# Optimization experiments

Measured on AMD Instinct MI355X. Metric: run time of the kernel, lower is better.

Reference implementation:

```python
import jax, jax.numpy as jnp
import numpy as np

EMBED_DIM = 1024
NUM_HEADS = 16
HEAD_DIM = EMBED_DIM // NUM_HEADS


def setup_inputs() -> dict:
    key = jax.random.key(0)
    k_x, k_wqkv, k_bqkv, k_wo, k_bo = jax.random.split(key, 5)
    b, n = 2, 2048
    scale_in = 1.0 / np.sqrt(EMBED_DIM)
    return {
        "x": jax.random.normal(k_x, (b, n, EMBED_DIM), dtype=jnp.float32),
        "W_qkv": jax.random.normal(k_wqkv, (EMBED_DIM, 3 * EMBED_DIM), dtype=jnp.float32) * scale_in,
        "b_qkv": jnp.zeros((3 * EMBED_DIM,), dtype=jnp.float32),
        "W_out": jax.random.normal(k_wo, (EMBED_DIM, EMBED_DIM), dtype=jnp.float32) * scale_in,
        "b_out": jnp.zeros((EMBED_DIM,), dtype=jnp.float32),
    }


def _rope_rotate(t, cos, sin):
    # t: [b, h, n, hd]; cos/sin: [1, 1, n, hd//2]
    t1, t2 = jnp.split(t, 2, axis=-1)
    return jnp.concatenate([cos * t1 - sin * t2, sin * t1 + cos * t2], axis=-1)


def reference(x, W_qkv, b_qkv, W_out, b_out):
    b, n, d = x.shape
    h, hd = NUM_HEADS, HEAD_DIM

    qkv = x @ W_qkv + b_qkv                      # [b, n, 3d]
    q, k, v = jnp.split(qkv, 3, axis=-1)
    q, k, v = [t.reshape(b, n, h, hd).transpose(0, 2, 1, 3) for t in (q, k, v)]

    # RoPE tables
    hd2 = hd // 2
    theta = 10000.0 ** (-2.0 * jnp.arange(hd2, dtype=jnp.float32) / hd)
    freqs = jnp.arange(n, dtype=jnp.float32)[:, None] * theta[None, :]  # [n, hd2]
    cos = jnp.cos(freqs)[None, None]
    sin = jnp.sin(freqs)[None, None]
    q = _rope_rotate(q, cos, sin)
    k = _rope_rotate(k, cos, sin)

    scores = jnp.einsum('bhqd,bhkd->bhqk', q, k) / jnp.sqrt(jnp.float32(hd))
    attn = jax.nn.softmax(scores, axis=-1)       # [b, h, n, n]
    out = jnp.einsum('bhqk,bhkd->bhqd', attn, v)
    out = out.transpose(0, 2, 1, 3).reshape(b, n, d)
    return out @ W_out + b_out
```

## Files before the change

kernel.cpp:

```cpp
#include <hip/hip_runtime.h>
#include <hip/hip_bf16.h>
#include <math.h>

#define EMBED 1024
#define NHEAD 16
#define HD 64
#define BATCH 2
#define SEQ 2048
#define MTOT (BATCH * SEQ)
#define QKVN (3 * EMBED)

typedef __attribute__((ext_vector_type(8))) short short8;
typedef __attribute__((ext_vector_type(4))) float f32x4;

typedef __attribute__((address_space(1))) const unsigned int GUI;
typedef __attribute__((address_space(3))) unsigned int LUI;

__device__ __forceinline__ void gload_lds16(const void* src, void* dst) {
  __builtin_amdgcn_global_load_lds((GUI*)src, (LUI*)dst, 16, 0, 0);
}

__device__ __forceinline__ unsigned short f2bf(float f) {
  unsigned u = __builtin_bit_cast(unsigned, f);
  u += 0x7fffu + ((u >> 16) & 1u);
  return (unsigned short)(u >> 16);
}

__device__ __forceinline__ unsigned cvt_pk_bf16(float lo, float hi) {
  unsigned r;
  asm("v_cvt_pk_bf16_f32 %0, %1, %2" : "=v"(r) : "v"(lo), "v"(hi));
  return r;
}

#if __has_builtin(__builtin_amdgcn_exp2f)
#define EXP2(x) __builtin_amdgcn_exp2f(x)
#else
#define EXP2(x) __builtin_exp2f(x)
#endif

#define QSCALE 0.1803368801111191f


__global__ __launch_bounds__(256) void k_cvt(const float* __restrict__ in,
                                             unsigned short* __restrict__ out, int n4) {
  int i = blockIdx.x * 256 + threadIdx.x;
  if (i >= n4) return;
  float4 v = reinterpret_cast<const float4*>(in)[i];
  ushort4 o;
  o.x = f2bf(v.x); o.y = f2bf(v.y); o.z = f2bf(v.z); o.w = f2bf(v.w);
  reinterpret_cast<ushort4*>(out)[i] = o;
}

__global__ __launch_bounds__(256) void k_transpose_cvt(const float* __restrict__ W,
                                                       unsigned short* __restrict__ WT,
                                                       int K, int Ncols) {
  __shared__ float tile[32][33];
  int n0 = blockIdx.x * 32, k0 = blockIdx.y * 32;
  int tc = threadIdx.x & 31, tr = threadIdx.x >> 5;
  for (int i = 0; i < 4; i++) {
    int r = tr + i * 8;
    tile[r][tc] = W[(size_t)(k0 + r) * Ncols + n0 + tc];
  }
  __syncthreads();
  for (int i = 0; i < 4; i++) {
    int r = tr + i * 8;
    WT[(size_t)(n0 + r) * K + k0 + tc] = f2bf(tile[tc][r]);
  }
}

__global__ __launch_bounds__(256) void k_rope_tables(float* __restrict__ cosT,
                                                     float* __restrict__ sinT) {
  int idx = blockIdx.x * 256 + threadIdx.x;
  if (idx >= SEQ * 32) return;
  int pos = idx >> 5, i = idx & 31;
  float theta = __expf((float)i * -0.28782313662425575f);
  float f = (float)pos * theta;
  cosT[idx] = cosf(f);
  sinT[idx] = sinf(f);
}

__device__ __forceinline__ void gemm_mainloop(const unsigned short* __restrict__ A,
                                              const unsigned short* __restrict__ Bt,
                                              unsigned short* Al, unsigned short* Bl,
                                              size_t m0, size_t n0,
                                              int tid, int l15, int g, int wm, int wn,
                                              f32x4 acc[4][4]) {
  const int w = tid >> 6;
  const int lane = tid & 63;
  const int srow = lane >> 3, slot = lane & 7;
  for (int k0 = 0; k0 < 1024; k0 += 64) {
    __syncthreads();
    for (int it = 0; it < 4; it++) {
      const int r = w * 32 + it * 8 + srow;
      const int sc = (slot ^ (r & 7)) * 8;
      gload_lds16(A + (m0 + r) * 1024 + k0 + sc, &Al[(w * 32 + it * 8) * 64]);
      gload_lds16(Bt + (n0 + r) * 1024 + k0 + sc, &Bl[(w * 32 + it * 8) * 64]);
    }
    __syncthreads();
    for (int kk = 0; kk < 2; kk++) {
      short8 fa[4], fb[4];
      const int xr = ((kk * 4 + g) ^ (l15 & 7)) * 8;
      for (int i = 0; i < 4; i++)
        fa[i] = *reinterpret_cast<const short8*>(&Al[(wm * 64 + i * 16 + l15) * 64 + xr]);
      for (int j = 0; j < 4; j++)
        fb[j] = *reinterpret_cast<const short8*>(&Bl[(wn * 64 + j * 16 + l15) * 64 + xr]);
      for (int i = 0; i < 4; i++)
        for (int j = 0; j < 4; j++)
          acc[i][j] = __builtin_amdgcn_mfma_f32_16x16x32_bf16(fa[i], fb[j], acc[i][j], 0, 0, 0);
    }
  }
}

__global__ __launch_bounds__(256) void k_qkv_gemm(const unsigned short* __restrict__ A,
                                                  const unsigned short* __restrict__ Bt,
                                                  const float* __restrict__ bias,
                                                  const float* __restrict__ cosT,
                                                  const float* __restrict__ sinT,
                                                  unsigned short* __restrict__ Qb,
                                                  unsigned short* __restrict__ Kb,
                                                  unsigned short* __restrict__ Vtg) {
  __shared__ alignas(16) unsigned short Al[128 * 64];
  __shared__ alignas(16) unsigned short Bl[128 * 64];
  const int tid = threadIdx.x;
  const int lane = tid & 63, l15 = lane & 15, g = lane >> 4;
  const int wid = tid >> 6, wm = wid >> 1, wn = wid & 1;
  const int bid = blockIdx.x;
  const int x = bid & 7, i6 = bid >> 3;
  const int nc = i6 >> 5, rr = i6 & 31;
  const int mp = x * 4 + (rr & 3);
  const int np = nc * 8 + (rr >> 2);
  const size_t m0 = (size_t)mp * 128;
  const size_t n0 = (size_t)np * 128;
  f32x4 acc[4][4] = {};
  gemm_mainloop(A, Bt, Al, Bl, m0, n0, tid, l15, g, wm, wn, acc);

  const int cbase = (int)n0 + wn * 64;
  const int sec = cbase >> 10;
  const int head = (cbase & 1023) >> 6;
  float bia[4];
  for (int j = 0; j < 4; j++) bia[j] = bias[cbase + j * 16 + l15];
  const size_t mw = m0 + wm * 64;

  if (sec == 2) {
    for (int i = 0; i < 4; i++) {
      size_t mbase = mw + i * 16 + g * 4;
      int bb = (int)(mbase >> 11), pos0 = (int)(mbase & 2047);
      int k0 = pos0 & 63;
      int col = (pos0 & ~63) | (k0 & 32) | (((k0 >> 2) & 3) << 3) | (((k0 >> 4) & 1) << 2);
      size_t hb = (size_t)(bb * NHEAD + head) * HD;
      for (int j = 0; j < 4; j++) {
        int d = j * 16 + l15;
        uint2 pk;
        pk.x = cvt_pk_bf16(acc[i][j][0] + bia[j], acc[i][j][1] + bia[j]);
        pk.y = cvt_pk_bf16(acc[i][j][2] + bia[j], acc[i][j][3] + bia[j]);
        *reinterpret_cast<uint2*>(Vtg + (hb + d) * SEQ + col) = pk;
      }
    }
  } else {
    unsigned short* dst = sec ? Kb : Qb;
    const float qs = sec ? 1.0f : QSCALE;
    for (int i = 0; i < 4; i++)
      for (int r = 0; r < 4; r++) {
        size_t m = mw + i * 16 + g * 4 + r;
        int bb = (int)(m >> 11), pos = (int)(m & 2047);
        size_t base = ((size_t)(bb * NHEAD + head) * SEQ + pos) * HD;
        const float* cr = cosT + pos * 32;
        const float* sr = sinT + pos * 32;
        for (int pl = 0; pl < 2; pl++) {
          int ii = pl * 16 + l15;
          float c = cr[ii], s = sr[ii];
          float lo = acc[i][pl][r] + bia[pl];
          float hi = acc[i][pl + 2][r] + bia[pl + 2];
          dst[base + ii]      = f2bf((c * lo - s * hi) * qs);
          dst[base + 32 + ii] = f2bf((s * lo + c * hi) * qs);
        }
      }
  }
}

__global__ __launch_bounds__(256) void k_out_gemm(const unsigned short* __restrict__ A,
                                                  const unsigned short* __restrict__ Bt,
                                                  const float* __restrict__ bias,
                                                  float* __restrict__ out) {
  __shared__ alignas(16) unsigned short Al[128 * 64];
  __shared__ alignas(16) unsigned short Bl[64 * 64];
  const int tid = threadIdx.x;
  const int lane = tid & 63, l15 = lane & 15, g = lane >> 4;
  const int wid = tid >> 6, wm = wid >> 1, wn = wid & 1;
  const int w = wid;
  const int srow = lane >> 3, slot = lane & 7;
  const int bid = blockIdx.x;
  const int tile = (bid & 7) * 64 + (bid >> 3);
  const size_t m0 = (size_t)(tile / 16) * 128;
  const size_t n0 = (size_t)(tile % 16) * 64;
  f32x4 acc[4][2] = {};

  for (int k0 = 0; k0 < 1024; k0 += 64) {
    __syncthreads();
    for (int it = 0; it < 4; it++) {
      const int r = w * 32 + it * 8 + srow;
      const int sc = (slot ^ (r & 7)) * 8;
      gload_lds16(A + (m0 + r) * 1024 + k0 + sc, &Al[(w * 32 + it * 8) * 64]);
    }
    for (int it = 0; it < 2; it++) {
      const int r = w * 16 + it * 8 + srow;
      const int sc = (slot ^ (r & 7)) * 8;
      gload_lds16(Bt + (n0 + r) * 1024 + k0 + sc, &Bl[(w * 16 + it * 8) * 64]);
    }
    __syncthreads();
    for (int kk = 0; kk < 2; kk++) {
      short8 fa[4], fb[2];
      const int xr = ((kk * 4 + g) ^ (l15 & 7)) * 8;
      for (int i = 0; i < 4; i++)
        fa[i] = *reinterpret_cast<const short8*>(&Al[(wm * 64 + i * 16 + l15) * 64 + xr]);
      for (int j = 0; j < 2; j++)
        fb[j] = *reinterpret_cast<const short8*>(&Bl[(wn * 32 + j * 16 + l15) * 64 + xr]);
      for (int i = 0; i < 4; i++)
        for (int j = 0; j < 2; j++)
          acc[i][j] = __builtin_amdgcn_mfma_f32_16x16x32_bf16(fa[i], fb[j], acc[i][j], 0, 0, 0);
    }
  }

  const int cbase = (int)n0 + wn * 32;
  const size_t mw = m0 + wm * 64;
  for (int i = 0; i < 4; i++)
    for (int r = 0; r < 4; r++) {
      size_t m = mw + i * 16 + g * 4 + r;
      for (int j = 0; j < 2; j++) {
        int col = cbase + j * 16 + l15;
        out[m * EMBED + col] = acc[i][j][r] + bias[col];
      }
    }
}

__global__ __launch_bounds__(256) void k_attn(const unsigned short* __restrict__ Q,
                                              const unsigned short* __restrict__ Kg,
                                              const unsigned short* __restrict__ Vtg,
                                              float* __restrict__ Opart,
                                              float* __restrict__ lpart) {
  __shared__ alignas(16) unsigned short Kt[2][64 * 64];
  __shared__ alignas(16) unsigned short Vt[2][64 * 64];
  const int tid = threadIdx.x, w = tid >> 6, lane = tid & 63;
  const int l15 = lane & 15, g = lane >> 4;
  const int srow = lane >> 3, slot = lane & 7;

  const int n = blockIdx.x;
  const int xcd = n & 7, m = n >> 3;
  const int qb = m & 15, z = m >> 4;
  const int sp = z & 1, bh = (z >> 1) * 8 + xcd;

  const unsigned short* Qp = Q + (size_t)bh * SEQ * HD;
  const unsigned short* Kp = Kg + (size_t)bh * SEQ * HD;
  const unsigned short* Vp = Vtg + (size_t)bh * HD * SEQ;
  const int q0 = qb * 128 + w * 32;

  short8 aq[2][2];
#pragma unroll
  for (int u = 0; u < 2; u++)
#pragma unroll
    for (int kk = 0; kk < 2; kk++)
      aq[u][kk] = *reinterpret_cast<const short8*>(
          Qp + (size_t)(q0 + u * 16 + l15) * HD + kk * 32 + g * 8);

  const int sr16 = w * 16 + srow;
  const int sc0 = (slot ^ (sr16 & 7)) * 8;
  const int kb0 = sp * 1024;

  const f32x4 z4 = {0.f, 0.f, 0.f, 0.f};
  f32x4 o[2][4] = {};
  float lrow[2] = {0.f, 0.f};

#define STAGE(tt, b)                                                             \
  do {                                                                           \
    const int kb_ = kb0 + (tt) * 64;                                             \
    gload_lds16(Kp + (size_t)(kb_ + sr16) * HD + sc0, &Kt[b][(w * 16) * 64]);    \
    gload_lds16(Vp + (size_t)sr16 * SEQ + kb_ + sc0, &Vt[b][(w * 16) * 64]);     \
    gload_lds16(Kp + (size_t)(kb_ + sr16 + 8) * HD + sc0,                        \
                &Kt[b][(w * 16 + 8) * 64]);                                      \
    gload_lds16(Vp + (size_t)(sr16 + 8) * SEQ + kb_ + sc0,                       \
                &Vt[b][(w * 16 + 8) * 64]);                                      \
  } while (0)

#define COMPUTE(cur)                                                             \
  do {                                                                           \
    const unsigned short* Ktc = Kt[cur];                                         \
    const unsigned short* Vtc = Vt[cur];                                         \
    f32x4 s[2][4];                                                               \
    {                                                                            \
      const int xr = (g ^ (l15 & 7)) * 8;                                        \
      _Pragma("unroll") for (int c = 0; c < 4; c++) {                            \
        short8 ak = *reinterpret_cast<const short8*>(&Ktc[(c * 16 + l15) * 64 + xr]); \
        s[0][c] = __builtin_amdgcn_mfma_f32_16x16x32_bf16(ak, aq[0][0], z4, 0, 0, 0); \
        s[1][c] = __builtin_amdgcn_mfma_f32_16x16x32_bf16(ak, aq[1][0], z4, 0, 0, 0); \
      }                                                                          \
    }                                                                            \
    {                                                                            \
      const int xr = ((4 + g) ^ (l15 & 7)) * 8;                                  \
      _Pragma("unroll") for (int c = 0; c < 4; c++) {                            \
        short8 ak = *reinterpret_cast<const short8*>(&Ktc[(c * 16 + l15) * 64 + xr]); \
        s[0][c] = __builtin_amdgcn_mfma_f32_16x16x32_bf16(ak, aq[0][1], s[0][c], 0, 0, 0); \
        s[1][c] = __builtin_amdgcn_mfma_f32_16x16x32_bf16(ak, aq[1][1], s[1][c], 0, 0, 0); \
      }                                                                          \
    }                                                                            \
    unsigned wpk[2][8];                                                          \
    _Pragma("unroll") for (int u = 0; u < 2; u++) {                              \
      float rs = 0.f;                                                            \
      _Pragma("unroll") for (int c = 0; c < 4; c++) {                            \
        float p0 = EXP2(s[u][c][0]);                                             \
        float p1 = EXP2(s[u][c][1]);                                             \
        float p2 = EXP2(s[u][c][2]);                                             \
        float p3 = EXP2(s[u][c][3]);                                             \
        rs += (p0 + p1) + (p2 + p3);                                             \
        wpk[u][2 * c]     = cvt_pk_bf16(p0, p1);                                 \
        wpk[u][2 * c + 1] = cvt_pk_bf16(p2, p3);                                 \
      }                                                                          \
      lrow[u] += rs;                                                             \
    }                                                                            \
    _Pragma("unroll") for (int kk = 0; kk < 2; kk++) {                           \
      const int xr = ((kk * 4 + g) ^ (l15 & 7)) * 8;                             \
      short8 pb0 = __builtin_bit_cast(short8,                                    \
          uint4{wpk[0][4 * kk], wpk[0][4 * kk + 1], wpk[0][4 * kk + 2], wpk[0][4 * kk + 3]}); \
      short8 pb1 = __builtin_bit_cast(short8,                                    \
          uint4{wpk[1][4 * kk], wpk[1][4 * kk + 1], wpk[1][4 * kk + 2], wpk[1][4 * kk + 3]}); \
      _Pragma("unroll") for (int c2 = 0; c2 < 4; c2++) {                         \
        short8 av = *reinterpret_cast<const short8*>(&Vtc[(c2 * 16 + l15) * 64 + xr]); \
        o[0][c2] = __builtin_amdgcn_mfma_f32_16x16x32_bf16(av, pb0, o[0][c2], 0, 0, 0); \
        o[1][c2] = __builtin_amdgcn_mfma_f32_16x16x32_bf16(av, pb1, o[1][c2], 0, 0, 0); \
      }                                                                          \
    }                                                                            \
  } while (0)

  STAGE(0, 0);

  for (int t = 0; t < 15; t++) {
    const int cur = t & 1;
    STAGE(t + 1, cur ^ 1);
    asm volatile("s_waitcnt vmcnt(4)" ::: "memory");
    __builtin_amdgcn_s_barrier();
    COMPUTE(cur);
    __builtin_amdgcn_s_barrier();
  }
  asm volatile("s_waitcnt vmcnt(0)" ::: "memory");
  __builtin_amdgcn_s_barrier();
  COMPUTE(1);

#undef STAGE
#undef COMPUTE

  const size_t ob = (size_t)(sp * 32 + bh) * SEQ * HD;
#pragma unroll
  for (int u = 0; u < 2; u++) {
    float l = lrow[u];
    l += __shfl_xor(l, 16, 64);
    l += __shfl_xor(l, 32, 64);
    const int pos = q0 + u * 16 + l15;
    if (g == 0) lpart[(size_t)(sp * 32 + bh) * SEQ + pos] = l;
    float* orow = Opart + ob + (size_t)pos * HD;
#pragma unroll
    for (int c2 = 0; c2 < 4; c2++)
      *reinterpret_cast<f32x4*>(orow + c2 * 16 + g * 4) = o[u][c2];
  }
}

__global__ __launch_bounds__(256) void k_merge(const float* __restrict__ Op,
                                               const float* __restrict__ lp,
                                               unsigned short* __restrict__ AO) {
  const int t = threadIdx.x;
  const int bh = blockIdx.x >> 5, pt = blockIdx.x & 31;
  const int pos = pt * 64 + (t >> 2), dc = (t & 3) * 16;
  const float* p0 = Op + ((size_t)bh * SEQ + pos) * HD + dc;
  const float* p1 = p0 + (size_t)32 * SEQ * HD;
  const float l = lp[(size_t)bh * SEQ + pos] + lp[(size_t)(32 + bh) * SEQ + pos];
  const float inv = 1.f / l;
  unsigned pk[8];
#pragma unroll
  for (int i = 0; i < 4; i++) {
    float4 a = reinterpret_cast<const float4*>(p0)[i];
    float4 b = reinterpret_cast<const float4*>(p1)[i];
    pk[2 * i]     = cvt_pk_bf16((a.x + b.x) * inv, (a.y + b.y) * inv);
    pk[2 * i + 1] = cvt_pk_bf16((a.z + b.z) * inv, (a.w + b.w) * inv);
  }
  const int bb = bh >> 4, h = bh & 15;
  unsigned short* dst = AO + ((size_t)bb * SEQ + pos) * EMBED + h * HD + dc;
  *reinterpret_cast<uint4*>(dst)     = uint4{pk[0], pk[1], pk[2], pk[3]};
  *reinterpret_cast<uint4*>(dst + 8) = uint4{pk[4], pk[5], pk[6], pk[7]};
}

extern "C" void kernel_launch(void* const* d_in, const int* in_sizes, int n_in,
                              void* d_out, int out_size, void* d_ws, size_t ws_size,
                              hipStream_t stream) {
  const float* x    = (const float*)d_in[0];
  const float* Wqkv = (const float*)d_in[1];
  const float* bqkv = (const float*)d_in[2];
  const float* Wout = (const float*)d_in[3];
  const float* bout = (const float*)d_in[4];
  float* out = (float*)d_out;

  char* ws = (char*)d_ws;
  size_t off = 0;
  auto carve = [&](size_t bytes) {
    char* p = ws + off;
    off += (bytes + 255) & ~(size_t)255;
    return p;
  };
  float* cosT           = (float*)carve((size_t)SEQ * 32 * 4);
  float* sinT           = (float*)carve((size_t)SEQ * 32 * 4);
  unsigned short* Xb    = (unsigned short*)carve((size_t)MTOT * EMBED * 2);
  unsigned short* WqkvT = (unsigned short*)carve((size_t)QKVN * EMBED * 2);
  unsigned short* WoT   = (unsigned short*)carve((size_t)EMBED * EMBED * 2);
  unsigned short* Qb    = (unsigned short*)carve((size_t)MTOT * EMBED * 2);
  unsigned short* Kb    = (unsigned short*)carve((size_t)MTOT * EMBED * 2);
  unsigned short* Vtg   = (unsigned short*)carve((size_t)MTOT * EMBED * 2);
  unsigned short* AO    = (unsigned short*)carve((size_t)MTOT * EMBED * 2);
  float* Opart          = (float*)carve((size_t)2 * 32 * HD * SEQ * 4);
  float* lpart          = (float*)carve((size_t)2 * 32 * SEQ * 4);

  k_cvt<<<(MTOT * EMBED / 4 + 255) / 256, 256, 0, stream>>>(x, Xb, MTOT * EMBED / 4);
  k_transpose_cvt<<<dim3(QKVN / 32, EMBED / 32), 256, 0, stream>>>(Wqkv, WqkvT, EMBED, QKVN);
  k_transpose_cvt<<<dim3(EMBED / 32, EMBED / 32), 256, 0, stream>>>(Wout, WoT, EMBED, EMBED);
  k_rope_tables<<<(SEQ * 32) / 256, 256, 0, stream>>>(cosT, sinT);

  k_qkv_gemm<<<dim3(768), 256, 0, stream>>>(Xb, WqkvT, bqkv, cosT, sinT, Qb, Kb, Vtg);
  k_attn<<<dim3(1024), 256, 0, stream>>>(Qb, Kb, Vtg, Opart, lpart);
  k_merge<<<dim3(1024), 256, 0, stream>>>(Opart, lpart, AO);
  k_out_gemm<<<dim3(512), 256, 0, stream>>>(AO, WoT, bout, out);
}
```

Baseline: 137.2 us.

## Merge prep kernels into one launch and store attention partials as bf16

Result: faster. 128.0 us, median of 3 (-6.7%).

```diff
diff --git a/kernel.cpp b/kernel.cpp
--- a/kernel.cpp
+++ b/kernel.cpp
@@ -26,6 +26,11 @@
   return (unsigned short)(u >> 16);
 }
 
+__device__ __forceinline__ float bf2f(unsigned short u) {
+  unsigned v = (unsigned)u << 16;
+  return __builtin_bit_cast(float, v);
+}
+
 __device__ __forceinline__ unsigned cvt_pk_bf16(float lo, float hi) {
   unsigned r;
   asm("v_cvt_pk_bf16_f32 %0, %1, %2" : "=v"(r) : "v"(lo), "v"(hi));
@@ -40,43 +45,55 @@
 
 #define QSCALE 0.1803368801111191f
 
-
-__global__ __launch_bounds__(256) void k_cvt(const float* __restrict__ in,
-                                             unsigned short* __restrict__ out, int n4) {
-  int i = blockIdx.x * 256 + threadIdx.x;
-  if (i >= n4) return;
-  float4 v = reinterpret_cast<const float4*>(in)[i];
-  ushort4 o;
-  o.x = f2bf(v.x); o.y = f2bf(v.y); o.z = f2bf(v.z); o.w = f2bf(v.w);
-  reinterpret_cast<ushort4*>(out)[i] = o;
-}
-
-__global__ __launch_bounds__(256) void k_transpose_cvt(const float* __restrict__ W,
-                                                       unsigned short* __restrict__ WT,
-                                                       int K, int Ncols) {
+__global__ __launch_bounds__(256) void k_prep(const float* __restrict__ x,
+                                              unsigned short* __restrict__ Xb,
+                                              const float* __restrict__ Wqkv,
+                                              unsigned short* __restrict__ WqkvT,
+                                              const float* __restrict__ Wout,
+                                              unsigned short* __restrict__ WoT,
+                                              float* __restrict__ cosT,
+                                              float* __restrict__ sinT) {
   __shared__ float tile[32][33];
-  int n0 = blockIdx.x * 32, k0 = blockIdx.y * 32;
-  int tc = threadIdx.x & 31, tr = threadIdx.x >> 5;
-  for (int i = 0; i < 4; i++) {
-    int r = tr + i * 8;
-    tile[r][tc] = W[(size_t)(k0 + r) * Ncols + n0 + tc];
-  }
-  __syncthreads();
-  for (int i = 0; i < 4; i++) {
-    int r = tr + i * 8;
-    WT[(size_t)(n0 + r) * K + k0 + tc] = f2bf(tile[tc][r]);
-  }
-}
-
-__global__ __launch_bounds__(256) void k_rope_tables(float* __restrict__ cosT,
-                                                     float* __restrict__ sinT) {
-  int idx = blockIdx.x * 256 + threadIdx.x;
-  if (idx >= SEQ * 32) return;
-  int pos = idx >> 5, i = idx & 31;
-  float theta = __expf((float)i * -0.28782313662425575f);
-  float f = (float)pos * theta;
-  cosT[idx] = cosf(f);
-  sinT[idx] = sinf(f);
+  const int bid = blockIdx.x, tid = threadIdx.x;
+  if (bid < 4096) {
+    int i = bid * 256 + tid;
+    float4 v = reinterpret_cast<const float4*>(x)[i];
+    ushort4 o;
+    o.x = f2bf(v.x); o.y = f2bf(v.y); o.z = f2bf(v.z); o.w = f2bf(v.w);
+    reinterpret_cast<ushort4*>(Xb)[i] = o;
+  } else if (bid < 8192) {
+    const float* W;
+    unsigned short* WT;
+    int n0, k0, Ncols;
+    if (bid < 7168) {
+      int idx = bid - 4096;
+      W = Wqkv; WT = WqkvT; Ncols = QKVN;
+      n0 = (idx % 96) * 32; k0 = (idx / 96) * 32;
+    } else {
+      int idx = bid - 7168;
+      W = Wout; WT = WoT; Ncols = EMBED;
+      n0 = (idx & 31) * 32; k0 = (idx >> 5) * 32;
+    }
+    const int tc = tid & 31, tr = tid >> 5;
+    for (int i = 0; i < 4; i++) {
+      int r = tr + i * 8;
+      tile[r][tc] = W[(size_t)(k0 + r) * Ncols + n0 + tc];
+    }
+    __syncthreads();
+    for (int i = 0; i < 4; i++) {
+      int r = tr + i * 8;
+      WT[(size_t)(n0 + r) * EMBED + k0 + tc] = f2bf(tile[tc][r]);
+    }
+  } else {
+    int idx = (bid - 8192) * 256 + tid;
+    if (idx < SEQ * 32) {
+      int pos = idx >> 5, i = idx & 31;
+      float theta = __expf((float)i * -0.28782313662425575f);
+      float f = (float)pos * theta;
+      cosT[idx] = cosf(f);
+      sinT[idx] = sinf(f);
+    }
+  }
 }
 
 __device__ __forceinline__ void gemm_mainloop(const unsigned short* __restrict__ A,
@@ -236,7 +253,7 @@
 __global__ __launch_bounds__(256) void k_attn(const unsigned short* __restrict__ Q,
                                               const unsigned short* __restrict__ Kg,
                                               const unsigned short* __restrict__ Vtg,
-                                              float* __restrict__ Opart,
+                                              unsigned short* __restrict__ Opart,
                                               float* __restrict__ lpart) {
   __shared__ alignas(16) unsigned short Kt[2][64 * 64];
   __shared__ alignas(16) unsigned short Vt[2][64 * 64];
@@ -355,30 +372,43 @@
     l += __shfl_xor(l, 32, 64);
     const int pos = q0 + u * 16 + l15;
     if (g == 0) lpart[(size_t)(sp * 32 + bh) * SEQ + pos] = l;
-    float* orow = Opart + ob + (size_t)pos * HD;
-#pragma unroll
-    for (int c2 = 0; c2 < 4; c2++)
-      *reinterpret_cast<f32x4*>(orow + c2 * 16 + g * 4) = o[u][c2];
-  }
-}
-
-__global__ __launch_bounds__(256) void k_merge(const float* __restrict__ Op,
+    unsigned short* orow = Opart + ob + (size_t)pos * HD;
+#pragma unroll
+    for (int c2 = 0; c2 < 4; c2++) {
+      uint2 pk;
+      pk.x = cvt_pk_bf16(o[u][c2][0], o[u][c2][1]);
+      pk.y = cvt_pk_bf16(o[u][c2][2], o[u][c2][3]);
+      *reinterpret_cast<uint2*>(orow + c2 * 16 + g * 4) = pk;
+    }
+  }
+}
+
+__global__ __launch_bounds__(256) void k_merge(const unsigned short* __restrict__ Op,
                                                const float* __restrict__ lp,
                                                unsigned short* __restrict__ AO) {
   const int t = threadIdx.x;
   const int bh = blockIdx.x >> 5, pt = blockIdx.x & 31;
   const int pos = pt * 64 + (t >> 2), dc = (t & 3) * 16;
-  const float* p0 = Op + ((size_t)bh * SEQ + pos) * HD + dc;
-  const float* p1 = p0 + (size_t)32 * SEQ * HD;
+  const unsigned short* p0 = Op + ((size_t)bh * SEQ + pos) * HD + dc;
+  const unsigned short* p1 = p0 + (size_t)32 * SEQ * HD;
   const float l = lp[(size_t)bh * SEQ + pos] + lp[(size_t)(32 + bh) * SEQ + pos];
   const float inv = 1.f / l;
+  short8 a0 = *reinterpret_cast<const short8*>(p0);
+  short8 a1 = *reinterpret_cast<const short8*>(p0 + 8);
+  short8 b0 = *reinterpret_cast<const short8*>(p1);
+  short8 b1 = *reinterpret_cast<const short8*>(p1 + 8);
   unsigned pk[8];
 #pragma unroll
   for (int i = 0; i < 4; i++) {
-    float4 a = reinterpret_cast<const float4*>(p0)[i];
-    float4 b = reinterpret_cast<const float4*>(p1)[i];
-    pk[2 * i]     = cvt_pk_bf16((a.x + b.x) * inv, (a.y + b.y) * inv);
-    pk[2 * i + 1] = cvt_pk_bf16((a.z + b.z) * inv, (a.w + b.w) * inv);
+    float s0 = bf2f((unsigned short)a0[2 * i])     + bf2f((unsigned short)b0[2 * i]);
+    float s1 = bf2f((unsigned short)a0[2 * i + 1]) + bf2f((unsigned short)b0[2 * i + 1]);
+    pk[i] = cvt_pk_bf16(s0 * inv, s1 * inv);
+  }
+#pragma unroll
+  for (int i = 0; i < 4; i++) {
+    float s0 = bf2f((unsigned short)a1[2 * i])     + bf2f((unsigned short)b1[2 * i]);
+    float s1 = bf2f((unsigned short)a1[2 * i + 1]) + bf2f((unsigned short)b1[2 * i + 1]);
+    pk[4 + i] = cvt_pk_bf16(s0 * inv, s1 * inv);
   }
   const int bb = bh >> 4, h = bh & 15;
   unsigned short* dst = AO + ((size_t)bb * SEQ + pos) * EMBED + h * HD + dc;
@@ -412,14 +442,10 @@
   unsigned short* Kb    = (unsigned short*)carve((size_t)MTOT * EMBED * 2);
   unsigned short* Vtg   = (unsigned short*)carve((size_t)MTOT * EMBED * 2);
   unsigned short* AO    = (unsigned short*)carve((size_t)MTOT * EMBED * 2);
-  float* Opart          = (float*)carve((size_t)2 * 32 * HD * SEQ * 4);
+  unsigned short* Opart = (unsigned short*)carve((size_t)2 * 32 * SEQ * HD * 2);
   float* lpart          = (float*)carve((size_t)2 * 32 * SEQ * 4);
 
-  k_cvt<<<(MTOT * EMBED / 4 + 255) / 256, 256, 0, stream>>>(x, Xb, MTOT * EMBED / 4);
-  k_transpose_cvt<<<dim3(QKVN / 32, EMBED / 32), 256, 0, stream>>>(Wqkv, WqkvT, EMBED, QKVN);
-  k_transpose_cvt<<<dim3(EMBED / 32, EMBED / 32), 256, 0, stream>>>(Wout, WoT, EMBED, EMBED);
-  k_rope_tables<<<(SEQ * 32) / 256, 256, 0, stream>>>(cosT, sinT);
-
+  k_prep<<<dim3(8448), 256, 0, stream>>>(x, Xb, Wqkv, WqkvT, Wout, WoT, cosT, sinT);
   k_qkv_gemm<<<dim3(768), 256, 0, stream>>>(Xb, WqkvT, bqkv, cosT, sinT, Qb, Kb, Vtg);
   k_attn<<<dim3(1024), 256, 0, stream>>>(Qb, Kb, Vtg, Opart, lpart);
   k_merge<<<dim3(1024), 256, 0, stream>>>(Opart, lpart, AO);
```
